# Kernel tuning notes

Measured on AMD Instinct MI355X. Metric: run time of the kernel, lower is better.

## Reference

```python
import jax, jax.numpy as jnp
import numpy as np

N_FFT = 512
HOP = 128
WIN = 512
LENGTH = 600  # hardcoded in the original forward


def _hann(n):
    # torch.hann_window default is periodic: 0.5*(1-cos(2*pi*i/n))
    i = jnp.arange(n, dtype=jnp.float32)
    return 0.5 * (1.0 - jnp.cos(2.0 * jnp.pi * i / n))


def setup_inputs() -> dict:
    key = jax.random.key(0)
    x = jax.random.normal(key, (8192, 1, 257, 6, 2), dtype=jnp.float32)
    return {"x": x}


def reference(x):
    B, C, F, T, D = x.shape  # C==1, F==n_fft//2+1, D==2
    # view(B, F, T, D) + view_as_complex
    spec = x[:, 0, :, :, 0] + 1j * x[:, 0, :, :, 1]          # [B, F, T] complex64
    # inverse real FFT per frame (torch.istft, normalized=False, onesided=True)
    frames = jnp.fft.irfft(spec.transpose(0, 2, 1), n=N_FFT, axis=-1)  # [B, T, n_fft]
    win = _hann(WIN)                                          # [n_fft] (win_length == n_fft)
    frames = frames * win                                     # synthesis windowing
    # overlap-add
    L = HOP * (T - 1) + N_FFT
    idx = jnp.arange(T)[:, None] * HOP + jnp.arange(N_FFT)[None, :]  # [T, n_fft]
    y = jnp.zeros((B, L), dtype=frames.dtype).at[:, idx].add(frames)  # [B, L]
    # window-square envelope normalization (COLA division)
    env = jnp.zeros((L,), dtype=frames.dtype).at[idx].add(win * win)  # [L]
    # center=True trim of n_fft//2, then length=600 crop
    start = N_FFT // 2
    sig = y[:, start:start + LENGTH] / env[start:start + LENGTH]       # [B, 600]
    return sig[:, None, :]                                    # unsqueeze(1) -> [B, 1, 600]
```

## Files before the change

### kernel.cpp

```cpp
#include <hip/hip_runtime.h>
#include <hip/hip_bf16.h>


#define NFFT   512
#define HOP    128
#define KDIM   3084
#define KP     3136
#define NOUT   600
#define NP     640
#define BM     64
#define BN     128
#define BK     64
#define KSTEPS (KP / BK)
#define LDA    72

#define NFRAG_K 98
#define FRAG_SH 512
#define WTOT    ((size_t)(NP / 16) * NFRAG_K * FRAG_SH)

typedef short s16x8 __attribute__((ext_vector_type(8)));
typedef float f32x4 __attribute__((ext_vector_type(4)));

static __device__ __forceinline__ unsigned short bf16_bits(float f) {
    __hip_bfloat16 b = __float2bfloat16(f);
    return *(unsigned short*)&b;
}

static __device__ __forceinline__ void lds_barrier() {
    asm volatile("s_waitcnt lgkmcnt(0)" ::: "memory");
    __builtin_amdgcn_s_barrier();
    asm volatile("" ::: "memory");
}

__global__ __launch_bounds__(256) void gen_W(unsigned short* __restrict__ Wt,
                                             float4* __restrict__ outZ,
                                             int nvec4) {
    __shared__ float costab[512];
    __shared__ __align__(16) unsigned short rowbuf[KP];
    const int l   = blockIdx.x;
    const int tid = threadIdx.x;
    const float w0 = 6.283185307179586f / 512.0f;

    for (int i = blockIdx.x * 256 + tid; i < nvec4; i += NP * 256)
        outZ[i] = make_float4(0.f, 0.f, 0.f, 0.f);

    *(int4*)(rowbuf + tid * 8) = make_int4(0, 0, 0, 0);
    if (tid < 136) *(int4*)(rowbuf + (256 + tid) * 8) = make_int4(0, 0, 0, 0);
    costab[tid]       = __cosf((float)tid * w0);
    costab[tid + 256] = __cosf((float)(tid + 256) * w0);
    __syncthreads();

    if (l < NOUT) {
        const int p = l + 256;
        float env = 0.0f;
#pragma unroll
        for (int tt = 0; tt < 6; ++tt) {
            int m = p - HOP * tt;
            if (m >= 0 && m < NFFT) {
                float w = 0.5f - 0.5f * costab[m];
                env += w * w;
            }
        }
        const float inv = 1.0f / (512.0f * env);
        for (int f = tid; f <= 256; f += 256) {
            float cf = (f == 0 || f == 256) ? 1.0f : 2.0f;
#pragma unroll
            for (int t = 0; t < 6; ++t) {
                int n = p - HOP * t;
                if (n >= 0 && n < NFFT) {
                    float w = 0.5f - 0.5f * costab[n];
                    float scale = cf * w * inv;
                    int a = (f * n) & 511;
                    float c = costab[a];
                    float s = costab[(a + 384) & 511];
                    rowbuf[f * 12 + t * 2 + 0] = bf16_bits(scale * c);
                    rowbuf[f * 12 + t * 2 + 1] = bf16_bits(-scale * s);
                }
            }
        }
    }
    __syncthreads();

    const int n16 = l >> 4, r = l & 15;
    for (int u = tid; u < 392; u += 256) {
        const int kc = u >> 2, q = u & 3;
        int4 val = *(const int4*)(rowbuf + kc * 32 + q * 8);
        *(int4*)(Wt + (((size_t)n16 * NFRAG_K + kc) * 64 + q * 16 + r) * 8) = val;
    }
}

__global__ __launch_bounds__(256, 4) void gemm_kernel(
        const float* __restrict__ X,
        const unsigned short* __restrict__ Wt,
        float* __restrict__ out) {
    __shared__ __align__(16) unsigned short As[2 * BM * LDA];

    const int tid = threadIdx.x;
    const int bid  = blockIdx.x;
    const int xcd  = bid & 7;
    const int rest = bid >> 3;
    const int mt   = xcd * 16 + rest / 10;
    const int sub  = rest % 10;
    const int nt   = sub >> 1;
    const int kidx = sub & 1;
    const int mBase = mt * BM;
    const int nBase = nt * BN;
    const int sBeg  = kidx ? 25 : 0;
    const int sEnd  = kidx ? KSTEPS : 25;

    const int lane = tid & 63;
    const int wave = tid >> 6;
    const int wm   = (wave & 1) * 32;
    const int wn   = (wave >> 1) * 64;
    const int lrow = lane & 15;
    const int quad = lane >> 4;

    const int aRow = tid >> 4, aU = tid & 15;
    const float* aPtr = X + (size_t)(mBase + aRow) * KDIM + sBeg * BK + aU * 4;
    const int aColBase = aU * 4;
    const size_t aRowStride = (size_t)16 * KDIM;

    const int n16base = nt * 8 + (wave >> 1) * 4;
    const unsigned short* wB0 = Wt + (size_t)n16base * NFRAG_K * FRAG_SH
                                   + (size_t)lane * 8;

    f32x4 acc[2][4];
#pragma unroll
    for (int i = 0; i < 2; ++i)
#pragma unroll
        for (int j = 0; j < 4; ++j) acc[i][j] = (f32x4){0.f, 0.f, 0.f, 0.f};

#define ISSUE_A(AV, s)                                                         \
    {                                                                          \
        const int k0_ = (s) * BK;                                              \
        _Pragma("unroll")                                                      \
        for (int p = 0; p < 4; ++p) {                                          \
            AV[p] = make_float4(0.f, 0.f, 0.f, 0.f);                           \
            if (k0_ + aColBase < KDIM)                                         \
                AV[p] = *(const float4*)(aPtr + (size_t)((s) - sBeg) * BK +    \
                                         p * aRowStride);                      \
        }                                                                      \
    }

#define ISSUE_B4(BV, s, ks)                                                    \
    {                                                                          \
        const size_t kc_ = (size_t)(2 * (s) + (ks));                           \
        _Pragma("unroll")                                                      \
        for (int j = 0; j < 4; ++j)                                            \
            BV[j] = *(const s16x8*)(const void*)(wB0 +                         \
                        ((size_t)j * NFRAG_K + kc_) * FRAG_SH);                \
    }

#define STAGE_A(AV, ABASE)                                                     \
    {                                                                          \
        _Pragma("unroll")                                                      \
        for (int p = 0; p < 4; ++p) {                                          \
            float4 v = AV[p];                                                  \
            unsigned long long pk = (unsigned long long)bf16_bits(v.x) |       \
                                    ((unsigned long long)bf16_bits(v.y) << 16) |\
                                    ((unsigned long long)bf16_bits(v.z) << 32) |\
                                    ((unsigned long long)bf16_bits(v.w) << 48); \
            *(unsigned long long*)(As + (ABASE) + (aRow + 16 * p) * LDA +      \
                                   aU * 4) = pk;                               \
        }                                                                      \
    }

#define COMPUTE_KS(ks, ABASE, BV)                                              \
    {                                                                          \
        const int koff = (ks) * 32 + quad * 8;                                 \
        s16x8 afr0 = *(const s16x8*)(const void*)(As + (ABASE) +               \
                         (wm + lrow) * LDA + koff);                            \
        s16x8 afr1 = *(const s16x8*)(const void*)(As + (ABASE) +               \
                         (wm + 16 + lrow) * LDA + koff);                       \
        _Pragma("unroll")                                                      \
        for (int j = 0; j < 4; ++j)                                            \
            acc[0][j] = __builtin_amdgcn_mfma_f32_16x16x32_bf16(               \
                afr0, BV[j], acc[0][j], 0, 0, 0);                              \
        _Pragma("unroll")                                                      \
        for (int j = 0; j < 4; ++j)                                            \
            acc[1][j] = __builtin_amdgcn_mfma_f32_16x16x32_bf16(               \
                afr1, BV[j], acc[1][j], 0, 0, 0);                              \
    }

    float4 avH[4];
    s16x8  bv0[4], bv1[4];
    ISSUE_A(avH, sBeg);
    ISSUE_B4(bv0, sBeg, 0);
    ISSUE_B4(bv1, sBeg, 1);
    STAGE_A(avH, 0);
    ISSUE_A(avH, sBeg + 1);
    lds_barrier();

    int ard = 0;
    for (int step = sBeg; step < sEnd; ++step) {
        const int awr = ard ^ (BM * LDA);
        if (step + 1 < sEnd) {
            STAGE_A(avH, awr);
            if (step + 2 < sEnd) ISSUE_A(avH, step + 2);
        }
        COMPUTE_KS(0, ard, bv0);
        if (step + 1 < sEnd) ISSUE_B4(bv0, step + 1, 0);
        COMPUTE_KS(1, ard, bv1);
        if (step + 1 < sEnd) ISSUE_B4(bv1, step + 1, 1);
        lds_barrier();
        ard = awr;
    }

#undef ISSUE_A
#undef ISSUE_B4
#undef STAGE_A
#undef COMPUTE_KS

#pragma unroll
    for (int i = 0; i < 2; ++i) {
#pragma unroll
        for (int j = 0; j < 4; ++j) {
            int gn = nBase + wn + j * 16 + lrow;
            if (gn < NOUT) {
#pragma unroll
                for (int r = 0; r < 4; ++r) {
                    int gm = mBase + wm + i * 16 + quad * 4 + r;
                    atomicAdd(out + (size_t)gm * NOUT + gn, acc[i][j][r]);
                }
            }
        }
    }
}

extern "C" void kernel_launch(void* const* d_in, const int* in_sizes, int n_in,
                              void* d_out, int out_size, void* d_ws, size_t ws_size,
                              hipStream_t stream) {
    const float* X = (const float*)d_in[0];
    unsigned short* W = (unsigned short*)d_ws;
    float* out = (float*)d_out;

    gen_W<<<dim3(NP), 256, 0, stream>>>(W, (float4*)d_out, out_size / 4);
    gemm_kernel<<<dim3(128 * 5 * 2), 256, 0, stream>>>(X, W, out);
}
```

Baseline: 234.5 us.

## Load A fragments directly from global into registers, drop LDS staging

Removes the shared-memory double buffer for the A operand. Each wave now reads its own MFMA A fragments straight from global memory as fp32 float4 pairs and converts them to bf16 in registers, with a two-deep register pipeline and a scalar tail for the last partial K chunk. This drops the LDS writes, LDS reads and per-step barriers. In exchange, waves sharing the same M rows reload the same A data from global/L2 (the two N-waves duplicate it), and each lane's load pattern is less coalesced, 32-byte segments strided by rows.

Measured after the change: 284.8 us. 1.21x slower.

```diff
diff --git a/kernel.cpp b/kernel.cpp
--- a/kernel.cpp
+++ b/kernel.cpp
@@ -10,9 +10,6 @@
 #define NP     640
 #define BM     64
 #define BN     128
-#define BK     64
-#define KSTEPS (KP / BK)
-#define LDA    72
 
 #define NFRAG_K 98
 #define FRAG_SH 512
@@ -26,10 +23,13 @@
     return *(unsigned short*)&b;
 }
 
-static __device__ __forceinline__ void lds_barrier() {
-    asm volatile("s_waitcnt lgkmcnt(0)" ::: "memory");
-    __builtin_amdgcn_s_barrier();
-    asm volatile("" ::: "memory");
+static __device__ __forceinline__ s16x8 cvt_frag(float4 lo, float4 hi) {
+    s16x8 r;
+    r[0] = (short)bf16_bits(lo.x); r[1] = (short)bf16_bits(lo.y);
+    r[2] = (short)bf16_bits(lo.z); r[3] = (short)bf16_bits(lo.w);
+    r[4] = (short)bf16_bits(hi.x); r[5] = (short)bf16_bits(hi.y);
+    r[6] = (short)bf16_bits(hi.z); r[7] = (short)bf16_bits(hi.w);
+    return r;
 }
 
 __global__ __launch_bounds__(256) void gen_W(unsigned short* __restrict__ Wt,
@@ -93,8 +93,6 @@
         const float* __restrict__ X,
         const unsigned short* __restrict__ Wt,
         float* __restrict__ out) {
-    __shared__ __align__(16) unsigned short As[2 * BM * LDA];
-
     const int tid = threadIdx.x;
     const int bid  = blockIdx.x;
     const int xcd  = bid & 7;
@@ -105,8 +103,6 @@
     const int kidx = sub & 1;
     const int mBase = mt * BM;
     const int nBase = nt * BN;
-    const int sBeg  = kidx ? 25 : 0;
-    const int sEnd  = kidx ? KSTEPS : 25;
 
     const int lane = tid & 63;
     const int wave = tid >> 6;
@@ -115,10 +111,9 @@
     const int lrow = lane & 15;
     const int quad = lane >> 4;
 
-    const int aRow = tid >> 4, aU = tid & 15;
-    const float* aPtr = X + (size_t)(mBase + aRow) * KDIM + sBeg * BK + aU * 4;
-    const int aColBase = aU * 4;
-    const size_t aRowStride = (size_t)16 * KDIM;
+    const float* aRow0 = X + (size_t)(mBase + wm + lrow) * KDIM;
+    const float* aRow1 = aRow0 + (size_t)16 * KDIM;
+    const int kq = quad * 8;
 
     const int n16base = nt * 8 + (wave >> 1) * 4;
     const unsigned short* wB0 = Wt + (size_t)n16base * NFRAG_K * FRAG_SH
@@ -130,86 +125,78 @@
 #pragma unroll
         for (int j = 0; j < 4; ++j) acc[i][j] = (f32x4){0.f, 0.f, 0.f, 0.f};
 
-#define ISSUE_A(AV, s)                                                         \
+#define LOADA(L0, H0, L1, H1, kc_)                                             \
     {                                                                          \
-        const int k0_ = (s) * BK;                                              \
-        _Pragma("unroll")                                                      \
-        for (int p = 0; p < 4; ++p) {                                          \
-            AV[p] = make_float4(0.f, 0.f, 0.f, 0.f);                           \
-            if (k0_ + aColBase < KDIM)                                         \
-                AV[p] = *(const float4*)(aPtr + (size_t)((s) - sBeg) * BK +    \
-                                         p * aRowStride);                      \
-        }                                                                      \
-    }
-
-#define ISSUE_B4(BV, s, ks)                                                    \
+        const int kb_ = (kc_) * 32 + kq;                                       \
+        L0 = *(const float4*)(aRow0 + kb_);                                    \
+        H0 = *(const float4*)(aRow0 + kb_ + 4);                                \
+        L1 = *(const float4*)(aRow1 + kb_);                                    \
+        H1 = *(const float4*)(aRow1 + kb_ + 4);                                \
+    }
+
+#define LOADB(BV, kc_)                                                         \
     {                                                                          \
-        const size_t kc_ = (size_t)(2 * (s) + (ks));                           \
         _Pragma("unroll")                                                      \
         for (int j = 0; j < 4; ++j)                                            \
             BV[j] = *(const s16x8*)(const void*)(wB0 +                         \
-                        ((size_t)j * NFRAG_K + kc_) * FRAG_SH);                \
-    }
-
-#define STAGE_A(AV, ABASE)                                                     \
+                        ((size_t)j * NFRAG_K + (size_t)(kc_)) * FRAG_SH);      \
+    }
+
+#define COMPUTE(L0, H0, L1, H1, BV)                                            \
     {                                                                          \
-        _Pragma("unroll")                                                      \
-        for (int p = 0; p < 4; ++p) {                                          \
-            float4 v = AV[p];                                                  \
-            unsigned long long pk = (unsigned long long)bf16_bits(v.x) |       \
-                                    ((unsigned long long)bf16_bits(v.y) << 16) |\
-                                    ((unsigned long long)bf16_bits(v.z) << 32) |\
-                                    ((unsigned long long)bf16_bits(v.w) << 48); \
-            *(unsigned long long*)(As + (ABASE) + (aRow + 16 * p) * LDA +      \
-                                   aU * 4) = pk;                               \
-        }                                                                      \
-    }
-
-#define COMPUTE_KS(ks, ABASE, BV)                                              \
-    {                                                                          \
-        const int koff = (ks) * 32 + quad * 8;                                 \
-        s16x8 afr0 = *(const s16x8*)(const void*)(As + (ABASE) +               \
-                         (wm + lrow) * LDA + koff);                            \
-        s16x8 afr1 = *(const s16x8*)(const void*)(As + (ABASE) +               \
-                         (wm + 16 + lrow) * LDA + koff);                       \
+        s16x8 af0 = cvt_frag(L0, H0);                                          \
+        s16x8 af1 = cvt_frag(L1, H1);                                          \
         _Pragma("unroll")                                                      \
         for (int j = 0; j < 4; ++j)                                            \
             acc[0][j] = __builtin_amdgcn_mfma_f32_16x16x32_bf16(               \
-                afr0, BV[j], acc[0][j], 0, 0, 0);                              \
+                af0, BV[j], acc[0][j], 0, 0, 0);                               \
         _Pragma("unroll")                                                      \
         for (int j = 0; j < 4; ++j)                                            \
             acc[1][j] = __builtin_amdgcn_mfma_f32_16x16x32_bf16(               \
-                afr1, BV[j], acc[1][j], 0, 0, 0);                              \
-    }
-
-    float4 avH[4];
+                af1, BV[j], acc[1][j], 0, 0, 0);                               \
+    }
+
+    const int kcBeg = kidx ? 50 : 0;
+    const int kcEnd = kidx ? 96 : 50;
+
+    float4 a0l0, a0h0, a1l0, a1h0;
+    float4 a0l1, a0h1, a1l1, a1h1;
     s16x8  bv0[4], bv1[4];
-    ISSUE_A(avH, sBeg);
-    ISSUE_B4(bv0, sBeg, 0);
-    ISSUE_B4(bv1, sBeg, 1);
-    STAGE_A(avH, 0);
-    ISSUE_A(avH, sBeg + 1);
-    lds_barrier();
-
-    int ard = 0;
-    for (int step = sBeg; step < sEnd; ++step) {
-        const int awr = ard ^ (BM * LDA);
-        if (step + 1 < sEnd) {
-            STAGE_A(avH, awr);
-            if (step + 2 < sEnd) ISSUE_A(avH, step + 2);
-        }
-        COMPUTE_KS(0, ard, bv0);
-        if (step + 1 < sEnd) ISSUE_B4(bv0, step + 1, 0);
-        COMPUTE_KS(1, ard, bv1);
-        if (step + 1 < sEnd) ISSUE_B4(bv1, step + 1, 1);
-        lds_barrier();
-        ard = awr;
-    }
-
-#undef ISSUE_A
-#undef ISSUE_B4
-#undef STAGE_A
-#undef COMPUTE_KS
+
+    LOADA(a0l0, a0h0, a1l0, a1h0, kcBeg);
+    LOADB(bv0, kcBeg);
+    for (int kc = kcBeg; kc + 1 < kcEnd; kc += 2) {
+        LOADA(a0l1, a0h1, a1l1, a1h1, kc + 1);
+        LOADB(bv1, kc + 1);
+        COMPUTE(a0l0, a0h0, a1l0, a1h0, bv0);
+        if (kc + 2 < kcEnd) {
+            LOADA(a0l0, a0h0, a1l0, a1h0, kc + 2);
+            LOADB(bv0, kc + 2);
+        }
+        COMPUTE(a0l1, a0h1, a1l1, a1h1, bv1);
+    }
+
+    if (kidx) {
+        const int kb = 96 * 32 + kq;
+        float e0[8], e1[8];
+#pragma unroll
+        for (int e = 0; e < 8; ++e) {
+            const int k = kb + e;
+            const bool ok = (k < KDIM);
+            e0[e] = ok ? aRow0[k] : 0.f;
+            e1[e] = ok ? aRow1[k] : 0.f;
+        }
+        float4 l0 = make_float4(e0[0], e0[1], e0[2], e0[3]);
+        float4 h0 = make_float4(e0[4], e0[5], e0[6], e0[7]);
+        float4 l1 = make_float4(e1[0], e1[1], e1[2], e1[3]);
+        float4 h1 = make_float4(e1[4], e1[5], e1[6], e1[7]);
+        LOADB(bv0, 96);
+        COMPUTE(l0, h0, l1, h1, bv0);
+    }
+
+#undef LOADA
+#undef LOADB
+#undef COMPUTE
 
 #pragma unroll
     for (int i = 0; i < 2; ++i) {
```
